# Kernel tuning notes

Hardware: AMD Instinct MI355X
Metric: run time of the kernel (lower is better)

## Reference

```python
import jax, jax.numpy as jnp
import numpy as np

POOL = 7        # adaptive max pool output size
STRIDE = 16.0   # feature stride of VGG16 conv5


def _bin_masks(lo, hi, size, nbins=POOL):
    """Boolean masks [R, nbins, size]: pixel p belongs to adaptive-pool bin i
    of the region [lo, hi). PyTorch AdaptiveMaxPool2d bin boundaries:
    start = floor(i*L/n), end = ceil((i+1)*L/n), L = hi - lo."""
    L = hi - lo                                   # [R]
    i = jnp.arange(nbins, dtype=jnp.int32)
    starts = lo[:, None] + (i[None, :] * L[:, None]) // nbins          # [R, nbins]
    ends = lo[:, None] + ((i[None, :] + 1) * L[:, None] + nbins - 1) // nbins
    pos = jnp.arange(size, dtype=jnp.int32)
    return (pos[None, None, :] >= starts[..., None]) & (pos[None, None, :] < ends[..., None])


def roi_pool(x, rois):
    """x: [1,C,H,W]; rois: [R,4] = (y1,x1,y2,x2) in image pixels.
    Returns [R, C, POOL, POOL], matching the per-ROI slice + AdaptiveMaxPool2d loop."""
    xf = x[0]                                     # [C,H,W]
    C, H, W = xf.shape
    h0 = (rois[:, 0] / STRIDE).astype(jnp.int32)
    h1 = (rois[:, 2] / STRIDE).astype(jnp.int32) + 1
    w0 = (rois[:, 1] / STRIDE).astype(jnp.int32)
    w1 = (rois[:, 3] / STRIDE).astype(jnp.int32) + 1
    mH = _bin_masks(h0, h1, H)                    # [R,7,H]
    mW = _bin_masks(w0, w1, W)                    # [R,7,W]
    NEG = jnp.finfo(xf.dtype).min
    # reduce over W per w-bin (small fixed loop over 7 bins keeps memory bounded)
    colmax = jnp.stack(
        [jnp.where(mW[:, wb][:, None, None, :], xf[None], NEG).max(-1) for wb in range(POOL)],
        axis=-1)                                  # [R,C,H,7]
    # reduce over H per h-bin
    pooled = jnp.stack(
        [jnp.where(mH[:, hb][:, None, :, None], colmax, NEG).max(2) for hb in range(POOL)],
        axis=2)                                   # [R,C,7,7]
    return pooled


def setup_inputs() -> dict:
    key = jax.random.key(0)
    ks = jax.random.split(key, 10)
    H_img, W_img = 16 * 37, 16 * 50
    x = jax.random.normal(ks[0], (1, 512, 37, 50), dtype=jnp.float32)
    R = 128
    y1 = jax.random.uniform(ks[1], (R,), minval=0.0, maxval=H_img - 32.0)
    x1 = jax.random.uniform(ks[2], (R,), minval=0.0, maxval=W_img - 32.0)
    hh = jax.random.uniform(ks[3], (R,), minval=16.0, maxval=256.0)
    ww = jax.random.uniform(ks[4], (R,), minval=16.0, maxval=256.0)
    y2 = jnp.minimum(y1 + hh, H_img - 1.0)
    x2 = jnp.minimum(x1 + ww, W_img - 1.0)
    rois = jnp.stack([y1, x1, y2, x2], axis=1).astype(jnp.float32)
    D_in, D_h = 512 * POOL * POOL, 4096
    n_class = 21
    W1 = jax.random.normal(ks[5], (D_in, D_h), dtype=jnp.float32) * 0.01
    b1 = jnp.zeros((D_h,), jnp.float32)
    W2 = jax.random.normal(ks[6], (D_h, D_h), dtype=jnp.float32) * 0.01
    b2 = jnp.zeros((D_h,), jnp.float32)
    Wloc = jax.random.normal(ks[7], (D_h, n_class * 4), dtype=jnp.float32) * 0.001
    bloc = jnp.zeros((n_class * 4,), jnp.float32)
    Wscore = jax.random.normal(ks[8], (D_h, n_class), dtype=jnp.float32) * 0.01
    bscore = jnp.zeros((n_class,), jnp.float32)
    return {"x": x, "rois": rois, "W1": W1, "b1": b1, "W2": W2, "b2": b2,
            "Wloc": Wloc, "bloc": bloc, "Wscore": Wscore, "bscore": bscore}


def reference(x, rois, W1, b1, W2, b2, Wloc, bloc, Wscore, bscore):
    pooled = roi_pool(x, rois)                    # [R,512,7,7]
    flat = pooled.reshape(pooled.shape[0], -1)    # [R,25088]
    fc6 = jax.nn.relu(flat @ W1 + b1)
    fc7 = jax.nn.relu(fc6 @ W2 + b2)
    roi_locs = fc7 @ Wloc + bloc                  # [R, n_class*4]
    roi_scores = fc7 @ Wscore + bscore            # [R, n_class]
    return roi_locs, roi_scores
```

## Files before the change

### kernel.cpp

```cpp
#include <hip/hip_runtime.h>
#include <hip/hip_bf16.h>


typedef __attribute__((ext_vector_type(8))) short bf16x8;
typedef __attribute__((ext_vector_type(4))) float f32x4;
typedef __attribute__((ext_vector_type(4))) short s16x4;

typedef const __attribute__((address_space(1))) void gvoid;
typedef __attribute__((address_space(3))) void lvoid;
#define GLD_LDS16(gp, lp) __builtin_amdgcn_global_load_lds((gvoid*)(gp), (lvoid*)(lp), 16, 0, 0)

static __device__ __forceinline__ short f2bf(float f) {
  unsigned u = __builtin_bit_cast(unsigned, f);
  u += 0x7fffu + ((u >> 16) & 1u);
  return (short)(u >> 16);
}

__global__ __launch_bounds__(256) void roipool_kernel(
    const float* __restrict__ x, const float* __restrict__ rois,
    __hip_bfloat16* __restrict__ A) {
  const int cg = blockIdx.x;
  const int r  = blockIdx.y;
  const float y1 = rois[r*4+0], x1 = rois[r*4+1], y2 = rois[r*4+2], x2 = rois[r*4+3];
  const int h0 = (int)(y1 * 0.0625f);
  const int h1 = (int)(y2 * 0.0625f) + 1;
  const int w0 = (int)(x1 * 0.0625f);
  const int w1 = (int)(x2 * 0.0625f) + 1;
  const int Hh = h1 - h0, Ww = w1 - w0;
  const int n = Hh * Ww;
  __shared__ float tile[16][292];
  const int cl = threadIdx.x >> 4, i = threadIdx.x & 15;
  const int c = cg*16 + cl;
  const float* xc = x + c*1850 + h0*50 + w0;
  for (int p = i; p < n; p += 16) {
    int rr = p / Ww, cc = p - rr*Ww;
    tile[cl][p] = xc[rr*50 + cc];
  }
  __syncthreads();
  __hip_bfloat16* Arow = A + (size_t)r*25088 + c*49;
  for (int b = i; b < 49; b += 16) {
    int hb = b / 7, wb = b - hb*7;
    int rs = (hb*Hh)/7,  re = ((hb+1)*Hh + 6)/7;
    int cs = (wb*Ww)/7,  ce = ((wb+1)*Ww + 6)/7;
    float m = -3.402823466e38f;
    for (int rr2 = rs; rr2 < re; ++rr2)
      for (int cc2 = cs; cc2 < ce; ++cc2)
        m = fmaxf(m, tile[cl][rr2*Ww + cc2]);
    Arow[b] = __float2bfloat16(m);
  }
}

__global__ __launch_bounds__(256) void gemm_kernel(
    const __hip_bfloat16* __restrict__ A,
    const float* __restrict__ B,
    float* __restrict__ part,
    int K, int KC) {
  __shared__ short lA[8192];
  __shared__ float lB[4096];
  const int t = threadIdx.x;
  const int w = t >> 6, l = t & 63;
  const int nb = blockIdx.x, s = blockIdx.y;
  const int kc0 = s * KC;
  const int Arow_bytes = K * 2;

  int aoff[4], boff[4];
#pragma unroll
  for (int p = 0; p < 4; ++p) {
    int o = (p*256 + t) * 16;
    int oa = o ^ (((o >> 7) & 7) << 4);
    aoff[p] = (oa >> 7) * Arow_bytes + (oa & 127);
    int ob = o ^ (((o >> 11) & 1) << 6);
    boff[p] = (ob >> 8) * 16384 + (ob & 255);
  }
  const int r15 = l & 15, kh = l >> 4;
  const int xa = (r15 & 7) << 4;
  const int aoj0 = r15*128 + ((kh*16) ^ xa);
  const int aoj1 = r15*128 + (((64) + kh*16) ^ xa);
  const int bo0  = ((kh*8)*256 + (w*16 + r15)*4) ^ ((kh & 1) << 6);

  const char* Ak = (const char*)A + kc0*2;
  const char* Bk = (const char*)B + (size_t)kc0*16384 + nb*256;

  f32x4 acc[8] = {};
  const int steps = KC >> 6;
  for (int st = 0; st < steps; ++st) {
    __syncthreads();
#pragma unroll
    for (int p = 0; p < 4; ++p) {
      GLD_LDS16(Ak + aoff[p], (char*)lA + (p*256 + w*64)*16);
      GLD_LDS16(Bk + boff[p], (char*)lB + (p*256 + w*64)*16);
    }
    __syncthreads();
#pragma unroll
    for (int j = 0; j < 2; ++j) {
      const int ao = j ? aoj1 : aoj0;
      const int bo = (j ? 8192 : 0) + bo0;
      float bf[8];
#pragma unroll
      for (int i2 = 0; i2 < 8; ++i2)
        bf[i2] = *(const float*)((const char*)lB + bo + i2*256);
      bf16x8 bfrag;
#pragma unroll
      for (int i2 = 0; i2 < 8; ++i2) bfrag[i2] = f2bf(bf[i2]);
#pragma unroll
      for (int mf = 0; mf < 8; ++mf) {
        bf16x8 afrag = *(const bf16x8*)((const char*)lA + mf*2048 + ao);
        acc[mf] = __builtin_amdgcn_mfma_f32_16x16x32_bf16(afrag, bfrag, acc[mf], 0, 0, 0);
      }
    }
    Ak += 128;
    Bk += 64 * 16384;
  }
  const int n = nb*64 + w*16 + r15;
  float* prow = part + (size_t)s*524288 + n;
#pragma unroll
  for (int mf = 0; mf < 8; ++mf) {
    int m0 = mf*16 + kh*4;
#pragma unroll
    for (int q = 0; q < 4; ++q)
      prow[(m0 + q)*4096] = acc[mf][q];
  }
}

template <int OUTF32>
__global__ __launch_bounds__(256) void reduce_kernel(
    const float* __restrict__ part, const float* __restrict__ bias,
    void* __restrict__ outp) {
  const int idx = (blockIdx.x*256 + threadIdx.x) * 4;
  f32x4 sum = {};
#pragma unroll
  for (int s2 = 0; s2 < 8; ++s2)
    sum += *(const f32x4*)(part + (size_t)s2*524288 + idx);
  sum += *(const f32x4*)(bias + (idx & 4095));
  if (OUTF32) {
    f32x4 o;
#pragma unroll
    for (int q = 0; q < 4; ++q) o[q] = fmaxf(sum[q], 0.f);
    *(f32x4*)((float*)outp + idx) = o;
  } else {
    s16x4 o;
#pragma unroll
    for (int q = 0; q < 4; ++q) o[q] = f2bf(fmaxf(sum[q], 0.f));
    *(s16x4*)((short*)outp + idx) = o;
  }
}

__global__ __launch_bounds__(512) void final_kernel(
    const float* __restrict__ fc7,
    const float* __restrict__ Wloc, const float* __restrict__ bloc,
    const float* __restrict__ Wscore, const float* __restrict__ bscore,
    float* __restrict__ out) {
  __shared__ float row[4096];
  __shared__ float psum[4][128];
  const int r = blockIdx.x, t = threadIdx.x;
  const float* src = fc7 + (size_t)r*4096;
  for (int i = t; i < 1024; i += 512)
    *(f32x4*)&row[i*4] = *(const f32x4*)&src[i*4];
  __syncthreads();
  const int c = t & 127, ks = t >> 7;
  float acc = 0.f;
  if (c < 105) {
    const float* W; int stride, cc;
    if (c < 84) { W = Wloc; stride = 84; cc = c; }
    else        { W = Wscore; stride = 21; cc = c - 84; }
    const int k0 = ks * 1024;
#pragma unroll 4
    for (int k = k0; k < k0 + 1024; ++k)
      acc = fmaf(row[k], W[(size_t)k*stride + cc], acc);
  }
  psum[ks][c] = acc;
  __syncthreads();
  if (ks == 0 && c < 105) {
    float v = psum[0][c] + psum[1][c] + psum[2][c] + psum[3][c];
    if (c < 84) out[(size_t)r*84 + c] = v + bloc[c];
    else        out[10752 + (size_t)r*21 + (c - 84)] = v + bscore[c - 84];
  }
}

extern "C" void kernel_launch(void* const* d_in, const int* in_sizes, int n_in,
                              void* d_out, int out_size, void* d_ws, size_t ws_size,
                              hipStream_t stream) {
  const float* x      = (const float*)d_in[0];
  const float* rois   = (const float*)d_in[1];
  const float* W1     = (const float*)d_in[2];
  const float* b1     = (const float*)d_in[3];
  const float* W2     = (const float*)d_in[4];
  const float* b2     = (const float*)d_in[5];
  const float* Wloc   = (const float*)d_in[6];
  const float* bloc   = (const float*)d_in[7];
  const float* Wscore = (const float*)d_in[8];
  const float* bscore = (const float*)d_in[9];
  float* out = (float*)d_out;

  char* ws = (char*)d_ws;
  __hip_bfloat16* Apool = (__hip_bfloat16*)(ws);
  short*          fc6   = (short*)(ws + 6422528);
  float*          fc7   = (float*)(ws + 7471104);
  float*          part  = (float*)(ws + 9568256);

  roipool_kernel<<<dim3(32, 128), 256, 0, stream>>>(x, rois, Apool);
  gemm_kernel<<<dim3(64, 8), 256, 0, stream>>>(Apool, W1, part, 25088, 3136);
  reduce_kernel<0><<<512, 256, 0, stream>>>(part, b1, (void*)fc6);
  gemm_kernel<<<dim3(64, 8), 256, 0, stream>>>((const __hip_bfloat16*)fc6, W2, part, 4096, 512);
  reduce_kernel<1><<<512, 256, 0, stream>>>(part, b2, (void*)fc7);
  final_kernel<<<128, 512, 0, stream>>>(fc7, Wloc, bloc, Wscore, bscore, out);
}
```

Measured before the change: 260.6 us.

## Double-buffer GEMM LDS tiles and remap block index so K-splits are adjacent

The GEMM kernel now uses two LDS buffers, so the global-to-LDS loads for the next K step are issued before the MFMAs on the current step, with explicit vmcnt waits and barriers in place of the two __syncthreads. This is meant to hide global memory latency behind compute in a kernel that streams W1 and is bandwidth bound. The grid is flattened, with the split index taken from the low bits of the block id, which changes block scheduling order so the eight K-splits of one N tile run together. LDS use doubles, which may reduce occupancy.

Measured after the change: 256.6 us. About the same (-1.5%).

```diff
diff --git a/kernel.cpp b/kernel.cpp
--- a/kernel.cpp
+++ b/kernel.cpp
@@ -9,6 +9,10 @@
 typedef const __attribute__((address_space(1))) void gvoid;
 typedef __attribute__((address_space(3))) void lvoid;
 #define GLD_LDS16(gp, lp) __builtin_amdgcn_global_load_lds((gvoid*)(gp), (lvoid*)(lp), 16, 0, 0)
+
+#define WAITV8() { asm volatile("s_waitcnt vmcnt(8)" ::: "memory"); __builtin_amdgcn_sched_barrier(0); }
+#define WAITV0() { asm volatile("s_waitcnt vmcnt(0)" ::: "memory"); __builtin_amdgcn_sched_barrier(0); }
+#define BAR() { __builtin_amdgcn_sched_barrier(0); __builtin_amdgcn_s_barrier(); __builtin_amdgcn_sched_barrier(0); }
 
 static __device__ __forceinline__ short f2bf(float f) {
   unsigned u = __builtin_bit_cast(unsigned, f);
@@ -55,11 +59,13 @@
     const float* __restrict__ B,
     float* __restrict__ part,
     int K, int KC) {
-  __shared__ short lA[8192];
-  __shared__ float lB[4096];
+  __shared__ short lA[2][8192];
+  __shared__ float lB[2][4096];
   const int t = threadIdx.x;
   const int w = t >> 6, l = t & 63;
-  const int nb = blockIdx.x, s = blockIdx.y;
+  const int bid = blockIdx.x;
+  const int s  = bid & 7;
+  const int nb = bid >> 3;
   const int kc0 = s * KC;
   const int Arow_bytes = K * 2;
 
@@ -83,14 +89,32 @@
 
   f32x4 acc[8] = {};
   const int steps = KC >> 6;
+  int cur = 0;
+
+#pragma unroll
+  for (int p = 0; p < 4; ++p) {
+    GLD_LDS16(Ak + aoff[p], (char*)lA[0] + (p*256 + w*64)*16);
+    GLD_LDS16(Bk + boff[p], (char*)lB[0] + (p*256 + w*64)*16);
+  }
+  Ak += 128; Bk += 64 * 16384;
+
   for (int st = 0; st < steps; ++st) {
-    __syncthreads();
-#pragma unroll
-    for (int p = 0; p < 4; ++p) {
-      GLD_LDS16(Ak + aoff[p], (char*)lA + (p*256 + w*64)*16);
-      GLD_LDS16(Bk + boff[p], (char*)lB + (p*256 + w*64)*16);
+    if (st + 1 < steps) {
+      char* dA = (char*)lA[cur ^ 1];
+      char* dB = (char*)lB[cur ^ 1];
+#pragma unroll
+      for (int p = 0; p < 4; ++p) {
+        GLD_LDS16(Ak + aoff[p], dA + (p*256 + w*64)*16);
+        GLD_LDS16(Bk + boff[p], dB + (p*256 + w*64)*16);
+      }
+      Ak += 128; Bk += 64 * 16384;
+      WAITV8();
+    } else {
+      WAITV0();
     }
-    __syncthreads();
+    BAR();
+    const char* lAb = (const char*)lA[cur];
+    const char* lBb = (const char*)lB[cur];
 #pragma unroll
     for (int j = 0; j < 2; ++j) {
       const int ao = j ? aoj1 : aoj0;
@@ -98,18 +122,18 @@
       float bf[8];
 #pragma unroll
       for (int i2 = 0; i2 < 8; ++i2)
-        bf[i2] = *(const float*)((const char*)lB + bo + i2*256);
+        bf[i2] = *(const float*)(lBb + bo + i2*256);
       bf16x8 bfrag;
 #pragma unroll
       for (int i2 = 0; i2 < 8; ++i2) bfrag[i2] = f2bf(bf[i2]);
 #pragma unroll
       for (int mf = 0; mf < 8; ++mf) {
-        bf16x8 afrag = *(const bf16x8*)((const char*)lA + mf*2048 + ao);
+        bf16x8 afrag = *(const bf16x8*)(lAb + mf*2048 + ao);
         acc[mf] = __builtin_amdgcn_mfma_f32_16x16x32_bf16(afrag, bfrag, acc[mf], 0, 0, 0);
       }
     }
-    Ak += 128;
-    Bk += 64 * 16384;
+    BAR();
+    cur ^= 1;
   }
   const int n = nb*64 + w*16 + r15;
   float* prow = part + (size_t)s*524288 + n;
@@ -199,9 +223,9 @@
   float*          part  = (float*)(ws + 9568256);
 
   roipool_kernel<<<dim3(32, 128), 256, 0, stream>>>(x, rois, Apool);
-  gemm_kernel<<<dim3(64, 8), 256, 0, stream>>>(Apool, W1, part, 25088, 3136);
+  gemm_kernel<<<512, 256, 0, stream>>>(Apool, W1, part, 25088, 3136);
   reduce_kernel<0><<<512, 256, 0, stream>>>(part, b1, (void*)fc6);
-  gemm_kernel<<<dim3(64, 8), 256, 0, stream>>>((const __hip_bfloat16*)fc6, W2, part, 4096, 512);
+  gemm_kernel<<<512, 256, 0, stream>>>((const __hip_bfloat16*)fc6, W2, part, 4096, 512);
   reduce_kernel<1><<<512, 256, 0, stream>>>(part, b2, (void*)fc7);
   final_kernel<<<128, 512, 0, stream>>>(fc7, Wloc, bloc, Wscore, bscore, out);
 }
```

## Fuse ROI head into one persistent kernel with grid barriers and double-buffered GEMM

Applied to the files above, without the earlier changes.

Replaces the six launches (roipool, two GEMMs, two reductions, final projection) with a single persistent kernel of 256 blocks synchronised by atomic grid barriers. The GEMM tile becomes 512 threads with double-buffered LDS loads issued through global_load_lds, overlapping the next K step's loads with MFMA work. The fc7 reduction is folded into the final projection. This removes launch gaps and overlaps memory with compute, but relies on all 256 blocks being co-resident and makes each block run two GEMM tiles in sequence.

Measured after the change: 463.1 us. +77.7%, slower.

```diff
diff --git a/kernel.cpp b/kernel.cpp
--- a/kernel.cpp
+++ b/kernel.cpp
@@ -9,6 +9,12 @@
 typedef const __attribute__((address_space(1))) void gvoid;
 typedef __attribute__((address_space(3))) void lvoid;
 #define GLD_LDS16(gp, lp) __builtin_amdgcn_global_load_lds((gvoid*)(gp), (lvoid*)(lp), 16, 0, 0)
+
+#define WAITV4() { asm volatile("s_waitcnt vmcnt(4)" ::: "memory"); __builtin_amdgcn_sched_barrier(0); }
+#define WAITV0() { asm volatile("s_waitcnt vmcnt(0)" ::: "memory"); __builtin_amdgcn_sched_barrier(0); }
+#define BAR() { __builtin_amdgcn_sched_barrier(0); __builtin_amdgcn_s_barrier(); __builtin_amdgcn_sched_barrier(0); }
+
+__device__ int g_bar[8];
 
 static __device__ __forceinline__ short f2bf(float f) {
   unsigned u = __builtin_bit_cast(unsigned, f);
@@ -16,164 +22,213 @@
   return (short)(u >> 16);
 }
 
-__global__ __launch_bounds__(256) void roipool_kernel(
-    const float* __restrict__ x, const float* __restrict__ rois,
-    __hip_bfloat16* __restrict__ A) {
-  const int cg = blockIdx.x;
-  const int r  = blockIdx.y;
-  const float y1 = rois[r*4+0], x1 = rois[r*4+1], y2 = rois[r*4+2], x2 = rois[r*4+3];
-  const int h0 = (int)(y1 * 0.0625f);
-  const int h1 = (int)(y2 * 0.0625f) + 1;
-  const int w0 = (int)(x1 * 0.0625f);
-  const int w1 = (int)(x2 * 0.0625f) + 1;
-  const int Hh = h1 - h0, Ww = w1 - w0;
-  const int n = Hh * Ww;
-  __shared__ float tile[16][292];
-  const int cl = threadIdx.x >> 4, i = threadIdx.x & 15;
-  const int c = cg*16 + cl;
-  const float* xc = x + c*1850 + h0*50 + w0;
-  for (int p = i; p < n; p += 16) {
-    int rr = p / Ww, cc = p - rr*Ww;
-    tile[cl][p] = xc[rr*50 + cc];
-  }
+static __device__ __forceinline__ void gridbar(int idx) {
   __syncthreads();
-  __hip_bfloat16* Arow = A + (size_t)r*25088 + c*49;
-  for (int b = i; b < 49; b += 16) {
-    int hb = b / 7, wb = b - hb*7;
-    int rs = (hb*Hh)/7,  re = ((hb+1)*Hh + 6)/7;
-    int cs = (wb*Ww)/7,  ce = ((wb+1)*Ww + 6)/7;
-    float m = -3.402823466e38f;
-    for (int rr2 = rs; rr2 < re; ++rr2)
-      for (int cc2 = cs; cc2 < ce; ++cc2)
-        m = fmaxf(m, tile[cl][rr2*Ww + cc2]);
-    Arow[b] = __float2bfloat16(m);
-  }
-}
-
-__global__ __launch_bounds__(256) void gemm_kernel(
-    const __hip_bfloat16* __restrict__ A,
-    const float* __restrict__ B,
-    float* __restrict__ part,
-    int K, int KC) {
-  __shared__ short lA[8192];
-  __shared__ float lB[4096];
+  if (threadIdx.x == 0) {
+    __threadfence();
+    __hip_atomic_fetch_add(&g_bar[idx], 1, __ATOMIC_ACQ_REL, __HIP_MEMORY_SCOPE_AGENT);
+    while (__hip_atomic_load(&g_bar[idx], __ATOMIC_ACQUIRE, __HIP_MEMORY_SCOPE_AGENT) < 256)
+      __builtin_amdgcn_s_sleep(8);
+    __threadfence();
+  }
+  __syncthreads();
+}
+
+static __device__ void gemm_tile(const short* __restrict__ A, const float* __restrict__ B,
+                                 float* __restrict__ part, int K, int KC, int steps,
+                                 int tid, char* smem) {
   const int t = threadIdx.x;
   const int w = t >> 6, l = t & 63;
-  const int nb = blockIdx.x, s = blockIdx.y;
-  const int kc0 = s * KC;
-  const int Arow_bytes = K * 2;
-
-  int aoff[4], boff[4];
-#pragma unroll
-  for (int p = 0; p < 4; ++p) {
-    int o = (p*256 + t) * 16;
+  const int wn = w & 3, wm = w >> 2;
+  const int s = tid & 7, nb = tid >> 3;
+  const int kc0 = s * KC, n0 = nb * 64;
+
+  int aoff[2], boff[2];
+#pragma unroll
+  for (int p = 0; p < 2; ++p) {
+    int o = (t + p*512) * 16;
     int oa = o ^ (((o >> 7) & 7) << 4);
-    aoff[p] = (oa >> 7) * Arow_bytes + (oa & 127);
+    aoff[p] = (oa >> 7) * (K*2) + (oa & 127);
     int ob = o ^ (((o >> 11) & 1) << 6);
     boff[p] = (ob >> 8) * 16384 + (ob & 255);
   }
   const int r15 = l & 15, kh = l >> 4;
   const int xa = (r15 & 7) << 4;
   const int aoj0 = r15*128 + ((kh*16) ^ xa);
-  const int aoj1 = r15*128 + (((64) + kh*16) ^ xa);
-  const int bo0  = ((kh*8)*256 + (w*16 + r15)*4) ^ ((kh & 1) << 6);
+  const int aoj1 = r15*128 + ((64 + kh*16) ^ xa);
+  const int bo0  = (kh*8*256 + (wn*16 + r15)*4) ^ ((kh & 1) << 6);
 
   const char* Ak = (const char*)A + kc0*2;
-  const char* Bk = (const char*)B + (size_t)kc0*16384 + nb*256;
-
-  f32x4 acc[8] = {};
-  const int steps = KC >> 6;
+  const char* Bk = (const char*)B + (size_t)kc0*16384 + n0*4;
+  char* const bA[2] = { smem,         smem + 32768 };
+  char* const bB[2] = { smem + 16384, smem + 49152 };
+
+  f32x4 acc[4] = {};
+  int cur = 0;
+#pragma unroll
+  for (int p = 0; p < 2; ++p) {
+    GLD_LDS16(Ak + aoff[p], bA[0] + (w*64 + p*512)*16);
+    GLD_LDS16(Bk + boff[p], bB[0] + (w*64 + p*512)*16);
+  }
+  Ak += 128; Bk += (size_t)64*16384;
+
   for (int st = 0; st < steps; ++st) {
-    __syncthreads();
-#pragma unroll
-    for (int p = 0; p < 4; ++p) {
-      GLD_LDS16(Ak + aoff[p], (char*)lA + (p*256 + w*64)*16);
-      GLD_LDS16(Bk + boff[p], (char*)lB + (p*256 + w*64)*16);
-    }
-    __syncthreads();
+    if (st + 1 < steps) {
+      char* dA = bA[cur^1]; char* dB = bB[cur^1];
+#pragma unroll
+      for (int p = 0; p < 2; ++p) {
+        GLD_LDS16(Ak + aoff[p], dA + (w*64 + p*512)*16);
+        GLD_LDS16(Bk + boff[p], dB + (w*64 + p*512)*16);
+      }
+      Ak += 128; Bk += (size_t)64*16384;
+      WAITV4();
+    } else {
+      WAITV0();
+    }
+    BAR();
+    const char* lAb = bA[cur]; const char* lBb = bB[cur];
 #pragma unroll
     for (int j = 0; j < 2; ++j) {
-      const int ao = j ? aoj1 : aoj0;
-      const int bo = (j ? 8192 : 0) + bo0;
+      const int ao = (j ? aoj1 : aoj0) + wm*8192;
+      const int bo = j*8192 + bo0;
       float bf[8];
 #pragma unroll
-      for (int i2 = 0; i2 < 8; ++i2)
-        bf[i2] = *(const float*)((const char*)lB + bo + i2*256);
+      for (int i2 = 0; i2 < 8; ++i2) bf[i2] = *(const float*)(lBb + bo + i2*256);
       bf16x8 bfrag;
 #pragma unroll
       for (int i2 = 0; i2 < 8; ++i2) bfrag[i2] = f2bf(bf[i2]);
 #pragma unroll
-      for (int mf = 0; mf < 8; ++mf) {
-        bf16x8 afrag = *(const bf16x8*)((const char*)lA + mf*2048 + ao);
+      for (int mf = 0; mf < 4; ++mf) {
+        bf16x8 afrag = *(const bf16x8*)(lAb + mf*2048 + ao);
         acc[mf] = __builtin_amdgcn_mfma_f32_16x16x32_bf16(afrag, bfrag, acc[mf], 0, 0, 0);
       }
     }
-    Ak += 128;
-    Bk += 64 * 16384;
-  }
-  const int n = nb*64 + w*16 + r15;
+    BAR();
+    cur ^= 1;
+  }
+  const int n = n0 + wn*16 + r15;
   float* prow = part + (size_t)s*524288 + n;
 #pragma unroll
-  for (int mf = 0; mf < 8; ++mf) {
-    int m0 = mf*16 + kh*4;
+  for (int mf = 0; mf < 4; ++mf) {
+    int m0 = (wm*4 + mf)*16 + kh*4;
 #pragma unroll
     for (int q = 0; q < 4; ++q)
       prow[(m0 + q)*4096] = acc[mf][q];
   }
 }
 
-template <int OUTF32>
-__global__ __launch_bounds__(256) void reduce_kernel(
-    const float* __restrict__ part, const float* __restrict__ bias,
-    void* __restrict__ outp) {
-  const int idx = (blockIdx.x*256 + threadIdx.x) * 4;
-  f32x4 sum = {};
-#pragma unroll
-  for (int s2 = 0; s2 < 8; ++s2)
-    sum += *(const f32x4*)(part + (size_t)s2*524288 + idx);
-  sum += *(const f32x4*)(bias + (idx & 4095));
-  if (OUTF32) {
-    f32x4 o;
-#pragma unroll
-    for (int q = 0; q < 4; ++q) o[q] = fmaxf(sum[q], 0.f);
-    *(f32x4*)((float*)outp + idx) = o;
-  } else {
+extern "C" __global__ void __launch_bounds__(512)
+fused_roihead(const float* __restrict__ x, const float* __restrict__ rois,
+              const float* __restrict__ W1, const float* __restrict__ b1,
+              const float* __restrict__ W2, const float* __restrict__ b2,
+              const float* __restrict__ Wloc, const float* __restrict__ bloc,
+              const float* __restrict__ Wscore, const float* __restrict__ bscore,
+              short* __restrict__ Apool, short* __restrict__ fc6,
+              float* __restrict__ part, float* __restrict__ out) {
+  __shared__ char smem[65536];
+  const int t = threadIdx.x, b = blockIdx.x;
+
+  {
+    float* tile = (float*)smem;
+    const int sub = t >> 8, cl = (t >> 4) & 15, i = t & 15;
+    float* tl = tile + (sub*16 + cl)*292;
+    for (int it = 0; it < 8; ++it) {
+      const int unit = it*512 + b*2 + sub;
+      const int r = unit >> 5, cg = unit & 31;
+      const int c = cg*16 + cl;
+      const float y1 = rois[r*4+0], x1 = rois[r*4+1], y2 = rois[r*4+2], x2 = rois[r*4+3];
+      const int h0 = (int)(y1*0.0625f), h1 = (int)(y2*0.0625f) + 1;
+      const int w0 = (int)(x1*0.0625f), w1 = (int)(x2*0.0625f) + 1;
+      const int Hh = h1-h0, Ww = w1-w0, n = Hh*Ww;
+      const float* xc = x + c*1850 + h0*50 + w0;
+      for (int p = i; p < n; p += 16) {
+        int rr = p / Ww, cc = p - rr*Ww;
+        tl[p] = xc[rr*50 + cc];
+      }
+      __syncthreads();
+      short* Arow = Apool + (size_t)r*25088 + c*49;
+      for (int bb = i; bb < 49; bb += 16) {
+        int hb = bb / 7, wb = bb - hb*7;
+        int rs = (hb*Hh)/7, re = ((hb+1)*Hh + 6)/7;
+        int cs = (wb*Ww)/7, ce = ((wb+1)*Ww + 6)/7;
+        float m = -3.402823466e38f;
+        for (int rr = rs; rr < re; ++rr)
+          for (int cc = cs; cc < ce; ++cc)
+            m = fmaxf(m, tl[rr*Ww + cc]);
+        Arow[bb] = f2bf(m);
+      }
+      __syncthreads();
+    }
+  }
+  gridbar(0);
+
+  gemm_tile(Apool, W1, part, 25088, 3136, 49, b,       smem);
+  gemm_tile(Apool, W1, part, 25088, 3136, 49, b + 256, smem);
+  gridbar(1);
+
+  {
+    const int idx = (b*512 + t) * 4;
+    f32x4 sum = {};
+#pragma unroll
+    for (int s2 = 0; s2 < 8; ++s2)
+      sum += *(const f32x4*)(part + (size_t)s2*524288 + idx);
+    sum += *(const f32x4*)(b1 + (idx & 4095));
     s16x4 o;
 #pragma unroll
     for (int q = 0; q < 4; ++q) o[q] = f2bf(fmaxf(sum[q], 0.f));
-    *(s16x4*)((short*)outp + idx) = o;
-  }
-}
-
-__global__ __launch_bounds__(512) void final_kernel(
-    const float* __restrict__ fc7,
-    const float* __restrict__ Wloc, const float* __restrict__ bloc,
-    const float* __restrict__ Wscore, const float* __restrict__ bscore,
-    float* __restrict__ out) {
-  __shared__ float row[4096];
-  __shared__ float psum[4][128];
-  const int r = blockIdx.x, t = threadIdx.x;
-  const float* src = fc7 + (size_t)r*4096;
-  for (int i = t; i < 1024; i += 512)
-    *(f32x4*)&row[i*4] = *(const f32x4*)&src[i*4];
+    *(s16x4*)(fc6 + idx) = o;
+  }
+  gridbar(2);
+
+  gemm_tile(fc6, W2, part, 4096, 512, 8, b,       smem);
+  gemm_tile(fc6, W2, part, 4096, 512, 8, b + 256, smem);
+  gridbar(3);
+
+  if (b < 128) {
+    float* row  = (float*)smem;
+    float* psum = (float*)(smem + 16384);
+    const int r = b;
+#pragma unroll
+    for (int ci = t; ci < 1024; ci += 512) {
+      f32x4 sum = {};
+#pragma unroll
+      for (int s2 = 0; s2 < 8; ++s2)
+        sum += *(const f32x4*)(part + (size_t)s2*524288 + r*4096 + ci*4);
+      sum += *(const f32x4*)(b2 + ci*4);
+      f32x4 o;
+#pragma unroll
+      for (int q = 0; q < 4; ++q) o[q] = fmaxf(sum[q], 0.f);
+      *(f32x4*)(row + ci*4) = o;
+    }
+    __syncthreads();
+    const int c = t & 127, ks = t >> 7;
+    float acc = 0.f;
+    if (c < 105) {
+      const float* W; int stride, cc;
+      if (c < 84) { W = Wloc; stride = 84; cc = c; }
+      else        { W = Wscore; stride = 21; cc = c - 84; }
+      const int k0 = ks * 1024;
+#pragma unroll 4
+      for (int k = k0; k < k0 + 1024; ++k)
+        acc = fmaf(row[k], W[(size_t)k*stride + cc], acc);
+    }
+    psum[ks*128 + c] = acc;
+    __syncthreads();
+    if (ks == 0 && c < 105) {
+      float v = psum[c] + psum[128+c] + psum[256+c] + psum[384+c];
+      if (c < 84) out[(size_t)r*84 + c] = v + bloc[c];
+      else        out[10752 + (size_t)r*21 + (c - 84)] = v + bscore[c - 84];
+    }
+  }
+
   __syncthreads();
-  const int c = t & 127, ks = t >> 7;
-  float acc = 0.f;
-  if (c < 105) {
-    const float* W; int stride, cc;
-    if (c < 84) { W = Wloc; stride = 84; cc = c; }
-    else        { W = Wscore; stride = 21; cc = c - 84; }
-    const int k0 = ks * 1024;
-#pragma unroll 4
-    for (int k = k0; k < k0 + 1024; ++k)
-      acc = fmaf(row[k], W[(size_t)k*stride + cc], acc);
-  }
-  psum[ks][c] = acc;
-  __syncthreads();
-  if (ks == 0 && c < 105) {
-    float v = psum[0][c] + psum[1][c] + psum[2][c] + psum[3][c];
-    if (c < 84) out[(size_t)r*84 + c] = v + bloc[c];
-    else        out[10752 + (size_t)r*21 + (c - 84)] = v + bscore[c - 84];
+  if (t == 0) {
+    int v = __hip_atomic_fetch_add(&g_bar[4], 1, __ATOMIC_ACQ_REL, __HIP_MEMORY_SCOPE_AGENT);
+    if (v == 255) {
+#pragma unroll
+      for (int i = 0; i < 5; ++i)
+        __hip_atomic_store(&g_bar[i], 0, __ATOMIC_RELAXED, __HIP_MEMORY_SCOPE_AGENT);
+    }
   }
 }
 
@@ -193,15 +248,11 @@
   float* out = (float*)d_out;
 
   char* ws = (char*)d_ws;
-  __hip_bfloat16* Apool = (__hip_bfloat16*)(ws);
-  short*          fc6   = (short*)(ws + 6422528);
-  float*          fc7   = (float*)(ws + 7471104);
-  float*          part  = (float*)(ws + 9568256);
-
-  roipool_kernel<<<dim3(32, 128), 256, 0, stream>>>(x, rois, Apool);
-  gemm_kernel<<<dim3(64, 8), 256, 0, stream>>>(Apool, W1, part, 25088, 3136);
-  reduce_kernel<0><<<512, 256, 0, stream>>>(part, b1, (void*)fc6);
-  gemm_kernel<<<dim3(64, 8), 256, 0, stream>>>((const __hip_bfloat16*)fc6, W2, part, 4096, 512);
-  reduce_kernel<1><<<512, 256, 0, stream>>>(part, b2, (void*)fc7);
-  final_kernel<<<128, 512, 0, stream>>>(fc7, Wloc, bloc, Wscore, bscore, out);
-}
+  short* Apool = (short*)(ws);
+  short* fc6   = (short*)(ws + 6422528);
+  float* part  = (float*)(ws + 9568256);
+
+  fused_roihead<<<256, 512, 0, stream>>>(x, rois, W1, b1, W2, b2,
+                                         Wloc, bloc, Wscore, bscore,
+                                         Apool, fc6, part, out);
+}
```
